# Performance work log

Measured on AMD Instinct MI355X. Metric: run time of the kernel, lower is better.

Reference implementation:

```python
import jax, jax.numpy as jnp
import numpy as np

WIDTHS = [2, 3, 5, 8, 13, 21, 34, 55, 89, 26]  # ragged one-hot feature widths, sum = 256
NSEG = len(WIDTHS)
B, IN = 8192, 256
LAYOUT = [1024, 1024, 1024, 256]
EPS = 1e-5  # BatchNorm1d default eps
TAU = 1.0


def setup_inputs() -> dict:
    key = jax.random.key(0)
    ks = iter(jax.random.split(key, 64))
    inp = {"x": jax.random.normal(next(ks), (B, IN), jnp.float32)}
    prev = IN
    for i, fc in enumerate(LAYOUT):
        inp[f"W{i}"] = jax.random.normal(next(ks), (fc, prev), jnp.float32) / np.float32(np.sqrt(prev))
        inp[f"b{i}"] = 0.01 * jax.random.normal(next(ks), (fc,), jnp.float32)
        if i + 1 < len(LAYOUT):  # Residual blocks carry BatchNorm params (eval mode)
            inp[f"g{i}"] = 1.0 + 0.1 * jax.random.normal(next(ks), (fc,), jnp.float32)
            inp[f"be{i}"] = 0.1 * jax.random.normal(next(ks), (fc,), jnp.float32)
            inp[f"rm{i}"] = 0.1 * jax.random.normal(next(ks), (fc,), jnp.float32)
            inp[f"rv{i}"] = 0.75 + 0.5 * jax.random.uniform(next(ks), (fc,), dtype=jnp.float32)
        prev += fc
    inp["seg_ids"] = jnp.asarray(np.repeat(np.arange(NSEG), WIDTHS), jnp.int32)  # [256]
    return inp


def _residual(x, W, b, g, be, rm, rv):
    # Linear -> eval-mode BatchNorm1d -> ReLU -> concat([out, input])
    h = x @ W.T + b
    h = (h - rm) * (g * jax.lax.rsqrt(rv + EPS)) + be
    return jnp.concatenate([jax.nn.relu(h), x], axis=1)


def _segment_softmax(x, seg_ids):
    # Fused segmented softmax over ragged feature groups (replaces per-feature Python loop)
    xt = x.T / TAU                                            # [F, B]
    m = jax.ops.segment_max(xt, seg_ids, num_segments=NSEG)   # [NSEG, B]
    e = jnp.exp(xt - m[seg_ids])
    s = jax.ops.segment_sum(e, seg_ids, num_segments=NSEG)
    return (e / s[seg_ids]).T                                 # [B, F]


def reference(x, W0, b0, g0, be0, rm0, rv0, W1, b1, g1, be1, rm1, rv1,
              W2, b2, g2, be2, rm2, rv2, W3, b3, seg_ids):
    h = _residual(x, W0, b0, g0, be0, rm0, rv0)   # [B, 1280]
    h = _residual(h, W1, b1, g1, be1, rm1, rv1)   # [B, 2304]
    h = _residual(h, W2, b2, g2, be2, rm2, rv2)   # [B, 3328]
    h = h @ W3.T + b3                              # [B, 256]
    return _segment_softmax(h, seg_ids)
```

## Files before the change

### kernel.cpp

```cpp
#include <hip/hip_runtime.h>
#include <hip/hip_fp16.h>


#define LDH 3328
#define NROWS 8192

typedef _Float16 f16x8 __attribute__((ext_vector_type(8)));
typedef _Float16 f16x4 __attribute__((ext_vector_type(4)));
typedef float f32x4 __attribute__((ext_vector_type(4)));

__constant__ int c_bnd[11] = {0, 2, 5, 10, 18, 31, 52, 86, 141, 230, 256};

__device__ __forceinline__ void async_cp16(const _Float16* g, _Float16* l) {
  __builtin_amdgcn_global_load_lds(
      (__attribute__((address_space(1))) void*)g,
      (__attribute__((address_space(3))) void*)l, 16, 0, 0);
}

__device__ __forceinline__ _Float16 f2h(float f) { return (_Float16)f; }

__global__ void cvt_kernel(const float* __restrict__ src,
                           _Float16* __restrict__ dst, int n4) {
  int i = blockIdx.x * blockDim.x + threadIdx.x;
  if (i >= n4) return;
  const float4 v = *(const float4*)&src[(size_t)i * 4];
  f16x4 h = {f2h(v.x), f2h(v.y), f2h(v.z), f2h(v.w)};
  *(f16x4*)&dst[(size_t)i * 4] = h;
}

__global__ void stagex_kernel(const float* __restrict__ x,
                              _Float16* __restrict__ H) {
  int i = blockIdx.x * blockDim.x + threadIdx.x;
  int row = i >> 6;
  int c = (i & 63) * 4;
  const float4 v = *(const float4*)&x[(size_t)row * 256 + c];
  f16x4 h = {f2h(v.x), f2h(v.y), f2h(v.z), f2h(v.w)};
  *(f16x4*)&H[(size_t)row * LDH + 3072 + c] = h;
}

template <int FUSE>
__launch_bounds__(256, 2) __global__
void gemm_kernel(const _Float16* __restrict__ A, int ldA, int K,
                 const _Float16* __restrict__ W,
                 const float* __restrict__ bias, const float* __restrict__ g,
                 const float* __restrict__ be, const float* __restrict__ rm,
                 const float* __restrict__ rv,
                 _Float16* __restrict__ outH, int outOff,
                 float* __restrict__ outF, int ldF) {
  __shared__ _Float16 Alds[128 * 64];
  __shared__ _Float16 Blds[128 * 64];

  const int tid = threadIdx.x;
  const int lane = tid & 63;
  const int wave = tid >> 6;
  const int wr = wave >> 1;
  const int wc = wave & 1;
  const int row0 = blockIdx.x * 128;
  const int col0 = blockIdx.y * 128;
  const int lr = lane >> 3;
  const int ls = lane & 7;
  const int lc = ls ^ lr;
  const int fr = lane & 15;
  const int q = lane >> 4;

  f32x4 acc[4][4] = {};

  for (int k0 = 0; k0 < K; k0 += 64) {
    __syncthreads();
#pragma unroll
    for (int it = 0; it < 4; ++it) {
      const int rl = it * 32 + wave * 8;
      const _Float16* ga =
          A + (size_t)(row0 + rl + lr) * ldA + k0 + lc * 8;
      async_cp16(ga, &Alds[rl * 64]);
      const _Float16* gb =
          W + (size_t)(col0 + rl + lr) * K + k0 + lc * 8;
      async_cp16(gb, &Blds[rl * 64]);
    }
    __syncthreads();

#pragma unroll
    for (int kq = 0; kq < 2; ++kq) {
      f16x8 av[4], bv[4];
#pragma unroll
      for (int t = 0; t < 4; ++t) {
        const int ra = wr * 64 + t * 16 + fr;
        av[t] = *(const f16x8*)&Alds[ra * 64 + (((q + 4 * kq) ^ (ra & 7)) * 8)];
        const int rb = wc * 64 + t * 16 + fr;
        bv[t] = *(const f16x8*)&Blds[rb * 64 + (((q + 4 * kq) ^ (rb & 7)) * 8)];
      }
#pragma unroll
      for (int tm = 0; tm < 4; ++tm)
#pragma unroll
        for (int tn = 0; tn < 4; ++tn)
          acc[tm][tn] = __builtin_amdgcn_mfma_f32_16x16x32_f16(
              av[tm], bv[tn], acc[tm][tn], 0, 0, 0);
    }
  }

#pragma unroll
  for (int tn = 0; tn < 4; ++tn) {
    const int n = col0 + wc * 64 + tn * 16 + fr;
    if constexpr (FUSE == 1) {
      const float alpha = g[n] * rsqrtf(rv[n] + 1e-5f);
      const float beta = (bias[n] - rm[n]) * alpha + be[n];
#pragma unroll
      for (int tm = 0; tm < 4; ++tm) {
        const int rbase = row0 + wr * 64 + tm * 16 + q * 4;
#pragma unroll
        for (int r = 0; r < 4; ++r) {
          float v = acc[tm][tn][r] * alpha + beta;
          v = fmaxf(v, 0.0f);
          outH[(size_t)(rbase + r) * LDH + outOff + n] = f2h(v);
        }
      }
    } else {
      const float bb = bias[n];
#pragma unroll
      for (int tm = 0; tm < 4; ++tm) {
        const int rbase = row0 + wr * 64 + tm * 16 + q * 4;
#pragma unroll
        for (int r = 0; r < 4; ++r)
          outF[(size_t)(rbase + r) * ldF + n] = acc[tm][tn][r] + bb;
      }
    }
  }
}

__global__ void segsoftmax_kernel(float* __restrict__ out,
                                  const int* __restrict__ segids) {
  __shared__ float vals[256];
  __shared__ float red[10];
  const int row = blockIdx.x;
  const int l = threadIdx.x;
  float4 v = *(float4*)&out[(size_t)row * 256 + l * 4];
  *(float4*)&vals[l * 4] = v;
  __syncthreads();
  if (l < 10) {
    float m = -1e30f;
    for (int j = c_bnd[l]; j < c_bnd[l + 1]; ++j) m = fmaxf(m, vals[j]);
    red[l] = m;
  }
  __syncthreads();
  const int4 s4 = *(const int4*)&segids[l * 4];
  float4 e;
  e.x = expf(v.x - red[s4.x]);
  e.y = expf(v.y - red[s4.y]);
  e.z = expf(v.z - red[s4.z]);
  e.w = expf(v.w - red[s4.w]);
  *(float4*)&vals[l * 4] = e;
  __syncthreads();
  if (l < 10) {
    float s = 0.0f;
    for (int j = c_bnd[l]; j < c_bnd[l + 1]; ++j) s += vals[j];
    red[l] = s;
  }
  __syncthreads();
  float4 o;
  o.x = e.x / red[s4.x];
  o.y = e.y / red[s4.y];
  o.z = e.z / red[s4.z];
  o.w = e.w / red[s4.w];
  *(float4*)&out[(size_t)row * 256 + l * 4] = o;
}

extern "C" void kernel_launch(void* const* d_in, const int* in_sizes, int n_in,
                              void* d_out, int out_size, void* d_ws,
                              size_t ws_size, hipStream_t stream) {
  const float* x = (const float*)d_in[0];
  const float* W0 = (const float*)d_in[1];
  const float* b0 = (const float*)d_in[2];
  const float* g0 = (const float*)d_in[3];
  const float* be0 = (const float*)d_in[4];
  const float* rm0 = (const float*)d_in[5];
  const float* rv0 = (const float*)d_in[6];
  const float* W1 = (const float*)d_in[7];
  const float* b1 = (const float*)d_in[8];
  const float* g1 = (const float*)d_in[9];
  const float* be1 = (const float*)d_in[10];
  const float* rm1 = (const float*)d_in[11];
  const float* rv1 = (const float*)d_in[12];
  const float* W2 = (const float*)d_in[13];
  const float* b2 = (const float*)d_in[14];
  const float* g2 = (const float*)d_in[15];
  const float* be2 = (const float*)d_in[16];
  const float* rm2 = (const float*)d_in[17];
  const float* rv2 = (const float*)d_in[18];
  const float* W3 = (const float*)d_in[19];
  const float* b3 = (const float*)d_in[20];
  const int* seg = (const int*)d_in[21];
  float* out = (float*)d_out;

  _Float16* H = (_Float16*)d_ws;
  size_t off = (size_t)NROWS * LDH;
  _Float16* Wh0 = H + off; off += 1024 * 256;
  _Float16* Wh1 = H + off; off += 1024 * 1280;
  _Float16* Wh2 = H + off; off += 1024 * 2304;
  _Float16* Wh3 = H + off;

  cvt_kernel<<<256, 256, 0, stream>>>(W0, Wh0, 65536);
  cvt_kernel<<<1280, 256, 0, stream>>>(W1, Wh1, 327680);
  cvt_kernel<<<2304, 256, 0, stream>>>(W2, Wh2, 589824);
  cvt_kernel<<<832, 256, 0, stream>>>(W3, Wh3, 212992);
  stagex_kernel<<<2048, 256, 0, stream>>>(x, H);

  dim3 blk(256);
  gemm_kernel<1><<<dim3(64, 8), blk, 0, stream>>>(
      H + 3072, LDH, 256, Wh0, b0, g0, be0, rm0, rv0, H, 2048, nullptr, 0);
  gemm_kernel<1><<<dim3(64, 8), blk, 0, stream>>>(
      H + 2048, LDH, 1280, Wh1, b1, g1, be1, rm1, rv1, H, 1024, nullptr, 0);
  gemm_kernel<1><<<dim3(64, 8), blk, 0, stream>>>(
      H + 1024, LDH, 2304, Wh2, b2, g2, be2, rm2, rv2, H, 0, nullptr, 0);
  gemm_kernel<0><<<dim3(64, 2), blk, 0, stream>>>(
      H, LDH, 3328, Wh3, b3, nullptr, nullptr, nullptr, nullptr, nullptr, 0,
      out, 256);
  segsoftmax_kernel<<<8192, 64, 0, stream>>>(out, seg);
}
```

Baseline: 272.9 us.

## Shrink GEMM tiles for more blocks, merge conversion kernels, batch softmax rows

```diff
diff --git a/kernel.cpp b/kernel.cpp
--- a/kernel.cpp
+++ b/kernel.cpp
@@ -19,27 +19,46 @@
 
 __device__ __forceinline__ _Float16 f2h(float f) { return (_Float16)f; }
 
-__global__ void cvt_kernel(const float* __restrict__ src,
-                           _Float16* __restrict__ dst, int n4) {
+__global__ void cvt_all_kernel(const float* __restrict__ s0,
+                               const float* __restrict__ s1,
+                               const float* __restrict__ s2,
+                               const float* __restrict__ s3,
+                               const float* __restrict__ x,
+                               _Float16* __restrict__ d0,
+                               _Float16* __restrict__ d1,
+                               _Float16* __restrict__ d2,
+                               _Float16* __restrict__ d3,
+                               _Float16* __restrict__ H,
+                               int n0, int n1, int n2, int n3, int n4) {
   int i = blockIdx.x * blockDim.x + threadIdx.x;
   if (i >= n4) return;
-  const float4 v = *(const float4*)&src[(size_t)i * 4];
+  if (i >= n3) {
+    const int j = i - n3;
+    const int row = j >> 6;
+    const int c = (j & 63) * 4;
+    const float4 v = *(const float4*)&x[(size_t)j * 4];
+    f16x4 h = {f2h(v.x), f2h(v.y), f2h(v.z), f2h(v.w)};
+    *(f16x4*)&H[(size_t)row * LDH + 3072 + c] = h;
+    return;
+  }
+  const float* s;
+  _Float16* d;
+  if (i < n0) {
+    s = s0; d = d0;
+  } else if (i < n1) {
+    s = s1 - (size_t)n0 * 4; d = d1 - (size_t)n0 * 4;
+  } else if (i < n2) {
+    s = s2 - (size_t)n1 * 4; d = d2 - (size_t)n1 * 4;
+  } else {
+    s = s3 - (size_t)n2 * 4; d = d3 - (size_t)n2 * 4;
+  }
+  const float4 v = *(const float4*)&s[(size_t)i * 4];
   f16x4 h = {f2h(v.x), f2h(v.y), f2h(v.z), f2h(v.w)};
-  *(f16x4*)&dst[(size_t)i * 4] = h;
-}
-
-__global__ void stagex_kernel(const float* __restrict__ x,
-                              _Float16* __restrict__ H) {
-  int i = blockIdx.x * blockDim.x + threadIdx.x;
-  int row = i >> 6;
-  int c = (i & 63) * 4;
-  const float4 v = *(const float4*)&x[(size_t)row * 256 + c];
-  f16x4 h = {f2h(v.x), f2h(v.y), f2h(v.z), f2h(v.w)};
-  *(f16x4*)&H[(size_t)row * LDH + 3072 + c] = h;
-}
-
-template <int FUSE>
-__launch_bounds__(256, 2) __global__
+  *(f16x4*)&d[(size_t)i * 4] = h;
+}
+
+template <int FUSE, int TN>
+__launch_bounds__(256, 4) __global__
 void gemm_kernel(const _Float16* __restrict__ A, int ldA, int K,
                  const _Float16* __restrict__ W,
                  const float* __restrict__ bias, const float* __restrict__ g,
@@ -47,66 +66,72 @@
                  const float* __restrict__ rv,
                  _Float16* __restrict__ outH, int outOff,
                  float* __restrict__ outF, int ldF) {
-  __shared__ _Float16 Alds[128 * 64];
-  __shared__ _Float16 Blds[128 * 64];
+  constexpr int BN = TN * 32;
+  __shared__ _Float16 Alds[64 * 64];
+  __shared__ _Float16 Blds[BN * 64];
 
   const int tid = threadIdx.x;
   const int lane = tid & 63;
   const int wave = tid >> 6;
   const int wr = wave >> 1;
   const int wc = wave & 1;
-  const int row0 = blockIdx.x * 128;
-  const int col0 = blockIdx.y * 128;
+  const int row0 = blockIdx.x * 64;
+  const int col0 = blockIdx.y * BN;
   const int lr = lane >> 3;
   const int ls = lane & 7;
   const int lc = ls ^ lr;
   const int fr = lane & 15;
   const int q = lane >> 4;
 
-  f32x4 acc[4][4] = {};
+  f32x4 acc[2][TN] = {};
 
   for (int k0 = 0; k0 < K; k0 += 64) {
     __syncthreads();
 #pragma unroll
-    for (int it = 0; it < 4; ++it) {
+    for (int it = 0; it < 2; ++it) {
       const int rl = it * 32 + wave * 8;
-      const _Float16* ga =
-          A + (size_t)(row0 + rl + lr) * ldA + k0 + lc * 8;
-      async_cp16(ga, &Alds[rl * 64]);
-      const _Float16* gb =
-          W + (size_t)(col0 + rl + lr) * K + k0 + lc * 8;
-      async_cp16(gb, &Blds[rl * 64]);
+      async_cp16(A + (size_t)(row0 + rl + lr) * ldA + k0 + lc * 8,
+                 &Alds[rl * 64]);
+    }
+#pragma unroll
+    for (int it = 0; it < TN; ++it) {
+      const int rl = it * 32 + wave * 8;
+      async_cp16(W + (size_t)(col0 + rl + lr) * K + k0 + lc * 8,
+                 &Blds[rl * 64]);
     }
     __syncthreads();
 
 #pragma unroll
     for (int kq = 0; kq < 2; ++kq) {
-      f16x8 av[4], bv[4];
-#pragma unroll
-      for (int t = 0; t < 4; ++t) {
-        const int ra = wr * 64 + t * 16 + fr;
+      f16x8 av[2], bv[TN];
+#pragma unroll
+      for (int t = 0; t < 2; ++t) {
+        const int ra = wr * 32 + t * 16 + fr;
         av[t] = *(const f16x8*)&Alds[ra * 64 + (((q + 4 * kq) ^ (ra & 7)) * 8)];
-        const int rb = wc * 64 + t * 16 + fr;
+      }
+#pragma unroll
+      for (int t = 0; t < TN; ++t) {
+        const int rb = wc * (TN * 16) + t * 16 + fr;
         bv[t] = *(const f16x8*)&Blds[rb * 64 + (((q + 4 * kq) ^ (rb & 7)) * 8)];
       }
 #pragma unroll
-      for (int tm = 0; tm < 4; ++tm)
-#pragma unroll
-        for (int tn = 0; tn < 4; ++tn)
+      for (int tm = 0; tm < 2; ++tm)
+#pragma unroll
+        for (int tn = 0; tn < TN; ++tn)
           acc[tm][tn] = __builtin_amdgcn_mfma_f32_16x16x32_f16(
               av[tm], bv[tn], acc[tm][tn], 0, 0, 0);
     }
   }
 
 #pragma unroll
-  for (int tn = 0; tn < 4; ++tn) {
-    const int n = col0 + wc * 64 + tn * 16 + fr;
+  for (int tn = 0; tn < TN; ++tn) {
+    const int n = col0 + wc * (TN * 16) + tn * 16 + fr;
     if constexpr (FUSE == 1) {
       const float alpha = g[n] * rsqrtf(rv[n] + 1e-5f);
       const float beta = (bias[n] - rm[n]) * alpha + be[n];
 #pragma unroll
-      for (int tm = 0; tm < 4; ++tm) {
-        const int rbase = row0 + wr * 64 + tm * 16 + q * 4;
+      for (int tm = 0; tm < 2; ++tm) {
+        const int rbase = row0 + wr * 32 + tm * 16 + q * 4;
 #pragma unroll
         for (int r = 0; r < 4; ++r) {
           float v = acc[tm][tn][r] * alpha + beta;
@@ -117,8 +142,8 @@
     } else {
       const float bb = bias[n];
 #pragma unroll
-      for (int tm = 0; tm < 4; ++tm) {
-        const int rbase = row0 + wr * 64 + tm * 16 + q * 4;
+      for (int tm = 0; tm < 2; ++tm) {
+        const int rbase = row0 + wr * 32 + tm * 16 + q * 4;
 #pragma unroll
         for (int r = 0; r < 4; ++r)
           outF[(size_t)(rbase + r) * ldF + n] = acc[tm][tn][r] + bb;
@@ -129,38 +154,39 @@
 
 __global__ void segsoftmax_kernel(float* __restrict__ out,
                                   const int* __restrict__ segids) {
-  __shared__ float vals[256];
-  __shared__ float red[10];
-  const int row = blockIdx.x;
-  const int l = threadIdx.x;
+  __shared__ float vals[4][256];
+  __shared__ float red[4][10];
+  const int w = threadIdx.x >> 6;
+  const int l = threadIdx.x & 63;
+  const int row = blockIdx.x * 4 + w;
   float4 v = *(float4*)&out[(size_t)row * 256 + l * 4];
-  *(float4*)&vals[l * 4] = v;
+  *(float4*)&vals[w][l * 4] = v;
   __syncthreads();
   if (l < 10) {
     float m = -1e30f;
-    for (int j = c_bnd[l]; j < c_bnd[l + 1]; ++j) m = fmaxf(m, vals[j]);
-    red[l] = m;
+    for (int j = c_bnd[l]; j < c_bnd[l + 1]; ++j) m = fmaxf(m, vals[w][j]);
+    red[w][l] = m;
   }
   __syncthreads();
   const int4 s4 = *(const int4*)&segids[l * 4];
   float4 e;
-  e.x = expf(v.x - red[s4.x]);
-  e.y = expf(v.y - red[s4.y]);
-  e.z = expf(v.z - red[s4.z]);
-  e.w = expf(v.w - red[s4.w]);
-  *(float4*)&vals[l * 4] = e;
+  e.x = expf(v.x - red[w][s4.x]);
+  e.y = expf(v.y - red[w][s4.y]);
+  e.z = expf(v.z - red[w][s4.z]);
+  e.w = expf(v.w - red[w][s4.w]);
+  *(float4*)&vals[w][l * 4] = e;
   __syncthreads();
   if (l < 10) {
     float s = 0.0f;
-    for (int j = c_bnd[l]; j < c_bnd[l + 1]; ++j) s += vals[j];
-    red[l] = s;
+    for (int j = c_bnd[l]; j < c_bnd[l + 1]; ++j) s += vals[w][j];
+    red[w][l] = s;
   }
   __syncthreads();
   float4 o;
-  o.x = e.x / red[s4.x];
-  o.y = e.y / red[s4.y];
-  o.z = e.z / red[s4.z];
-  o.w = e.w / red[s4.w];
+  o.x = e.x / red[w][s4.x];
+  o.y = e.y / red[w][s4.y];
+  o.z = e.z / red[w][s4.z];
+  o.w = e.w / red[w][s4.w];
   *(float4*)&out[(size_t)row * 256 + l * 4] = o;
 }
 
@@ -198,21 +224,20 @@
   _Float16* Wh2 = H + off; off += 1024 * 2304;
   _Float16* Wh3 = H + off;
 
-  cvt_kernel<<<256, 256, 0, stream>>>(W0, Wh0, 65536);
-  cvt_kernel<<<1280, 256, 0, stream>>>(W1, Wh1, 327680);
-  cvt_kernel<<<2304, 256, 0, stream>>>(W2, Wh2, 589824);
-  cvt_kernel<<<832, 256, 0, stream>>>(W3, Wh3, 212992);
-  stagex_kernel<<<2048, 256, 0, stream>>>(x, H);
+  const int n0 = 65536, n1 = n0 + 327680, n2 = n1 + 589824, n3 = n2 + 212992;
+  const int n4 = n3 + 524288;
+  cvt_all_kernel<<<(n4 + 255) / 256, 256, 0, stream>>>(
+      W0, W1, W2, W3, x, Wh0, Wh1, Wh2, Wh3, H, n0, n1, n2, n3, n4);
 
   dim3 blk(256);
-  gemm_kernel<1><<<dim3(64, 8), blk, 0, stream>>>(
+  gemm_kernel<1, 4><<<dim3(128, 8), blk, 0, stream>>>(
       H + 3072, LDH, 256, Wh0, b0, g0, be0, rm0, rv0, H, 2048, nullptr, 0);
-  gemm_kernel<1><<<dim3(64, 8), blk, 0, stream>>>(
+  gemm_kernel<1, 4><<<dim3(128, 8), blk, 0, stream>>>(
       H + 2048, LDH, 1280, Wh1, b1, g1, be1, rm1, rv1, H, 1024, nullptr, 0);
-  gemm_kernel<1><<<dim3(64, 8), blk, 0, stream>>>(
+  gemm_kernel<1, 4><<<dim3(128, 8), blk, 0, stream>>>(
       H + 1024, LDH, 2304, Wh2, b2, g2, be2, rm2, rv2, H, 0, nullptr, 0);
-  gemm_kernel<0><<<dim3(64, 2), blk, 0, stream>>>(
+  gemm_kernel<0, 2><<<dim3(128, 4), blk, 0, stream>>>(
       H, LDH, 3328, Wh3, b3, nullptr, nullptr, nullptr, nullptr, nullptr, 0,
       out, 256);
-  segsoftmax_kernel<<<8192, 64, 0, stream>>>(out, seg);
-}
+  segsoftmax_kernel<<<2048, 256, 0, stream>>>(out, seg);
+}
```

Result: faster. 256.7 us (-5.9%).
